# Kernel optimization log

Measured on AMD Instinct MI355X. Metric: run time of the kernel, lower is better.

## Reference

```python
import jax, jax.numpy as jnp
import numpy as np

M, NQ, NK, DX, H, HD, DT, KH = 2, 1024, 1024, 512, 8, 64, 2, 32
SCALE = HD ** -0.5


def setup_inputs() -> dict:
    key = jax.random.key(0)
    ks = jax.random.split(key, 12)
    w = lambda k, shape: jax.random.normal(k, shape, jnp.float32) * 0.02
    return dict(
        xq=jax.random.normal(ks[0], (M, NQ, DX), jnp.float32),
        xk=jax.random.normal(ks[1], (M, NK, DX), jnp.float32),
        xv=jax.random.normal(ks[2], (M, NK, DX), jnp.float32),
        tq=jax.random.normal(ks[3], (M, NQ, DT), jnp.float32),
        tk=jax.random.normal(ks[4], (M, NK, DT), jnp.float32),
        Wq=w(ks[5], (DX, H * HD)),
        Wk=w(ks[6], (DX, H * HD)),
        Wv=w(ks[7], (DX, H * HD)),
        Wo=w(ks[8], (H * HD, DX)),
        bo=jnp.zeros((DX,), jnp.float32),
        K1=w(ks[9], (DT, KH)),
        kb1=jnp.zeros((KH,), jnp.float32),
        K2=w(ks[10], (KH, H)),
        kb2=jnp.zeros((H,), jnp.float32),
    )


def _heads(t):
    # [b, n, h*d] -> [b, h, n, d]
    b, n, _ = t.shape
    return t.reshape(b, n, H, HD).transpose(0, 2, 1, 3)


def reference(xq, xk, xv, tq, tk, Wq, Wk, Wv, Wo, bo, K1, kb1, K2, kb2):
    q = _heads(xq @ Wq)            # [m,h,nq,d]
    k = _heads(xk @ Wk)            # [m,h,nk,d]
    token_dots = jnp.einsum('bhqd,bhkd->bhqk', q, k) * SCALE
    # diagonal attention term: query attends to its own (key/value-projected) token
    xq_k = _heads(xq @ Wk)
    diag_dots = jnp.sum(q * xq_k, axis=-1, keepdims=True) * SCALE   # [m,h,nq,1]
    token_dots = jnp.concatenate([token_dots, diag_dots], axis=-1)  # [m,h,nq,nk+1]
    # translation group action: pairwise differences, plus zero diagonal diff
    diff = tq[:, :, None, :] - tk[:, None, :, :]                    # [m,nq,nk,dt]
    diff = jnp.concatenate([diff, jnp.zeros((M, NQ, 1, DT), diff.dtype)], axis=2)
    # kernel network (MLP) -> per-head relative-position bias [m,nq,nk+1,h]
    kd = jax.nn.relu(diff @ K1 + kb1) @ K2 + kb2
    dots = token_dots + kd.transpose(0, 3, 1, 2)                    # [m,h,nq,nk+1]
    attn = jax.nn.softmax(dots, axis=-1)
    v = _heads(xv @ Wv)
    xq_v = _heads(xq @ Wv)
    out = jnp.einsum('bhqk,bhkd->bhqd', attn[..., :-1], v) + attn[..., -1:] * xq_v
    out = out.transpose(0, 2, 1, 3).reshape(M, NQ, H * HD) @ Wo + bo
    # phi_t is None -> tq_new = tq
    return (out, tq)
```

## Files before the change

kernel.cpp:

```cpp
#include <hip/hip_runtime.h>
#include <hip/hip_bf16.h>
#include <cstddef>

typedef __attribute__((ext_vector_type(8))) short bf16x8;
typedef __attribute__((ext_vector_type(4))) float f32x4;

constexpr int NH  = 8;
constexpr int HHD = 512;
constexpr int KHC = 32;
constexpr float SCALE_F = 0.125f;
constexpr int KSPLIT = 4;

__device__ __forceinline__ unsigned short f2bf(float f) {
    unsigned int u = __builtin_bit_cast(unsigned int, f);
    u = (u + 0x7FFFu + ((u >> 16) & 1u)) >> 16;
    return (unsigned short)u;
}
__device__ __forceinline__ float bf2f(unsigned short h) {
    unsigned int u = ((unsigned int)h) << 16;
    return __builtin_bit_cast(float, u);
}
__device__ __forceinline__ unsigned int cvt_pk_bf16(float lo, float hi) {
    unsigned int r;
    asm("v_cvt_pk_bf16_f32 %0, %1, %2" : "=v"(r) : "v"(lo), "v"(hi));
    return r;
}

struct PrepAll {
    const float* xs[3]; unsigned short* xd[3];
    const float* wsrc[4]; unsigned short* wdst[4];
    const float* tq; const float* tk;
    const float* K1; const float* kb1;
    float* Aa; float* Bb;
};
__global__ __launch_bounds__(256) void prep_all(PrepAll c) {
    __shared__ unsigned short Ts[64][66];
    const int b = blockIdx.x;
    const int t = threadIdx.x;

    if (b < 1536) {
        const int z = b / 512;
        const size_t i8 = ((size_t)(b - z * 512) * 256 + t) * 8;
        const float4 f0 = *(const float4*)(c.xs[z] + i8);
        const float4 f1 = *(const float4*)(c.xs[z] + i8 + 4);
        ushort4 o0, o1;
        o0.x = f2bf(f0.x); o0.y = f2bf(f0.y); o0.z = f2bf(f0.z); o0.w = f2bf(f0.w);
        o1.x = f2bf(f1.x); o1.y = f2bf(f1.y); o1.z = f2bf(f1.z); o1.w = f2bf(f1.w);
        *(ushort4*)(c.xd[z] + i8) = o0;
        *(ushort4*)(c.xd[z] + i8 + 4) = o1;
    } else if (b < 1792) {
        const int bb = b - 1536;
        const int z = bb >> 6;
        const int rem = bb & 63;
        const int k0 = (rem & 7) * 64, j0 = (rem >> 3) * 64;
        const float* W = c.wsrc[z];
        unsigned short* Wt = c.wdst[z];
        {
            const int kr = t >> 2;
            const int jc = (t & 3) * 16;
            const float* g = W + (size_t)(k0 + kr) * 512 + j0 + jc;
            #pragma unroll
            for (int i4 = 0; i4 < 4; ++i4) {
                float4 f = *(const float4*)(g + i4 * 4);
                Ts[kr][jc + i4 * 4 + 0] = f2bf(f.x);
                Ts[kr][jc + i4 * 4 + 1] = f2bf(f.y);
                Ts[kr][jc + i4 * 4 + 2] = f2bf(f.z);
                Ts[kr][jc + i4 * 4 + 3] = f2bf(f.w);
            }
        }
        __syncthreads();
        {
            const int j = t >> 2;
            const int kseg = (t & 3) * 16;
            unsigned short tmp[16];
            #pragma unroll
            for (int i = 0; i < 16; ++i) tmp[i] = Ts[kseg + i][j];
            unsigned short* g = Wt + (size_t)(j0 + j) * 512 + k0 + kseg;
            #pragma unroll
            for (int i4 = 0; i4 < 4; ++i4)
                *(ushort4*)(g + i4 * 4) = *(ushort4*)&tmp[i4 * 4];
        }
    } else {
        const int idx = (b - 1792) * 256 + t;
        const int which = idx >> 16;
        const int e = idx & 65535;
        const int row = e >> 5;
        const int j = e & 31;
        const float* tt = which ? c.tk : c.tq;
        float v = tt[row * 2 + 0] * c.K1[j] + tt[row * 2 + 1] * c.K1[KHC + j];
        if (!which) v += c.kb1[j];
        (which ? c.Bb : c.Aa)[e] = v;
    }
}

__device__ __forceinline__ void mfma_core_128(const unsigned short* __restrict__ A,
                                              const unsigned short* __restrict__ Bt,
                                              int r0, int c0, f32x4 acc[4][4])
{
    __shared__ __align__(16) char As[16384];
    __shared__ __align__(16) char Bs[16384];

    const int tid = threadIdx.x;
    const int l = tid & 63, w = tid >> 6;
    const int lw = l & 15, lg = l >> 4;
    const int wr = (w >> 1) * 64, wc = (w & 1) * 64;

    #pragma unroll
    for (int r = 0; r < 4; ++r)
        #pragma unroll
        for (int cb = 0; cb < 4; ++cb) acc[r][cb] = (f32x4){0.f, 0.f, 0.f, 0.f};

    const int row_s = tid >> 1;
    const int half  = tid & 1;

    for (int kb = 0; kb < 512; kb += 64) {
        __syncthreads();
        {
            const unsigned short* g = A + (size_t)(r0 + row_s) * 512 + kb + half * 32;
            const int base = row_s * 128 + half * 64;
            const int sw = (row_s & 7) << 4;
            #pragma unroll
            for (int i = 0; i < 4; ++i)
                *(float4*)(As + ((base + i * 16) ^ sw)) = *(const float4*)(g + i * 8);
        }
        {
            const unsigned short* g = Bt + (size_t)(c0 + row_s) * 512 + kb + half * 32;
            const int base = row_s * 128 + half * 64;
            const int sw = (row_s & 7) << 4;
            #pragma unroll
            for (int i = 0; i < 4; ++i)
                *(float4*)(Bs + ((base + i * 16) ^ sw)) = *(const float4*)(g + i * 8);
        }
        __syncthreads();

        bf16x8 bfrag[4][2];
        #pragma unroll
        for (int cb = 0; cb < 4; ++cb) {
            const int bcol = wc + cb * 16 + lw;
            const int sw = (bcol & 7) << 4;
            bfrag[cb][0] = *(const bf16x8*)(Bs + ((bcol * 128 + lg * 16) ^ sw));
            bfrag[cb][1] = *(const bf16x8*)(Bs + ((bcol * 128 + 64 + lg * 16) ^ sw));
        }
        #pragma unroll
        for (int r = 0; r < 4; ++r) {
            const int arow = wr + r * 16 + lw;
            const int sw = (arow & 7) << 4;
            bf16x8 a0 = *(const bf16x8*)(As + ((arow * 128 + lg * 16) ^ sw));
            bf16x8 a1 = *(const bf16x8*)(As + ((arow * 128 + 64 + lg * 16) ^ sw));
            #pragma unroll
            for (int cb = 0; cb < 4; ++cb) {
                acc[r][cb] = __builtin_amdgcn_mfma_f32_16x16x32_bf16(a0, bfrag[cb][0], acc[r][cb], 0, 0, 0);
                acc[r][cb] = __builtin_amdgcn_mfma_f32_16x16x32_bf16(a1, bfrag[cb][1], acc[r][cb], 0, 0, 0);
            }
        }
    }
}

struct ProjBias {
    const unsigned short* A[5];
    const unsigned short* B[5];
    unsigned short* O[5];
    unsigned short* VT;
    const float* Aa; const float* Bb;
    const float* K2; const float* kb2;
    unsigned short* kd;
};

__global__ __launch_bounds__(256) void projbias(ProjBias p) {
    const int b = blockIdx.x;
    const int tid = threadIdx.x;
    const int l = tid & 63;
    const int lw = l & 15, lg = l >> 4;

    if (b < 320) {
        const int z = b >> 6;
        const int t = b & 63;
        const int r0 = (t >> 2) * 128, c0 = (t & 3) * 128;
        f32x4 acc[4][4];
        mfma_core_128(p.A[z], p.B[z], r0, c0, acc);

        const int w = tid >> 6;
        const int wr = (w >> 1) * 64, wc = (w & 1) * 64;
        #pragma unroll
        for (int r = 0; r < 4; ++r)
            #pragma unroll
            for (int cb = 0; cb < 4; ++cb) {
                const int gc = c0 + wc + cb * 16 + lw;
                const int h = gc >> 6, d = gc & 63;
                #pragma unroll
                for (int rr = 0; rr < 4; ++rr) {
                    const int gr = r0 + wr + r * 16 + lg * 4 + rr;
                    const int m = gr >> 10, n = gr & 1023;
                    const unsigned short v = f2bf(acc[r][cb][rr]);
                    if (z == 2)
                        p.VT[(((size_t)m * NH + h) * 64 + d) * 1024 + n] = v;
                    else
                        p.O[z][(((size_t)m * NH + h) * 1024 + n) * 64 + d] = v;
                }
            }
    } else {
        const int bb = b - 320;
        const int kb = tid >> 6;
        const int kt = bb & 15;
        const int qg = (bb >> 4) & 63;
        const int m  = bb >> 10;

        float k2f[8];
        #pragma unroll
        for (int e = 0; e < 8; ++e)
            k2f[e] = (lw < 8) ? p.K2[(lg * 8 + e) * 8 + lw] : 0.f;
        union { unsigned int u[4]; bf16x8 v; } bu;
        #pragma unroll
        for (int i = 0; i < 4; ++i) bu.u[i] = cvt_pk_bf16(k2f[2 * i], k2f[2 * i + 1]);
        const bf16x8 bfrag = bu.v;

        const float c0v = (lw < 8) ? p.kb2[lw] : 0.f;
        const f32x4 cini = {c0v, c0v, c0v, c0v};

        const int kglob = kt * 64 + kb * 16 + lw;
        const float* bp = p.Bb + ((size_t)m * 1024 + kglob) * 32 + lg * 8;
        const float4 b0 = *(const float4*)bp;
        const float4 b1 = *(const float4*)(bp + 4);
        const float bl[8] = {b0.x, b0.y, b0.z, b0.w, b1.x, b1.y, b1.z, b1.w};

        const float* arow = p.Aa + ((size_t)m * 1024 + qg * 16) * 32 + lg * 8;
        unsigned short* kout = p.kd + (size_t)(m * 8 + lw) * 1048576
                             + qg * 16384 + kt * 1024 + kb * 256 + lg * 64;

        #pragma unroll
        for (int t = 0; t < 16; t += 2) {
            const float4 a00 = *(const float4*)(arow + (size_t)t * 32);
            const float4 a01 = *(const float4*)(arow + (size_t)t * 32 + 4);
            union { unsigned int u[4]; bf16x8 v; } r0u;
            r0u.u[0] = cvt_pk_bf16(fmaxf(a00.x - bl[0], 0.f), fmaxf(a00.y - bl[1], 0.f));
            r0u.u[1] = cvt_pk_bf16(fmaxf(a00.z - bl[2], 0.f), fmaxf(a00.w - bl[3], 0.f));
            r0u.u[2] = cvt_pk_bf16(fmaxf(a01.x - bl[4], 0.f), fmaxf(a01.y - bl[5], 0.f));
            r0u.u[3] = cvt_pk_bf16(fmaxf(a01.z - bl[6], 0.f), fmaxf(a01.w - bl[7], 0.f));
            const f32x4 d0 = __builtin_amdgcn_mfma_f32_16x16x32_bf16(r0u.v, bfrag, cini, 0, 0, 0);

            const float4 a10 = *(const float4*)(arow + (size_t)(t + 1) * 32);
            const float4 a11 = *(const float4*)(arow + (size_t)(t + 1) * 32 + 4);
            union { unsigned int u[4]; bf16x8 v; } r1u;
            r1u.u[0] = cvt_pk_bf16(fmaxf(a10.x - bl[0], 0.f), fmaxf(a10.y - bl[1], 0.f));
            r1u.u[1] = cvt_pk_bf16(fmaxf(a10.z - bl[2], 0.f), fmaxf(a10.w - bl[3], 0.f));
            r1u.u[2] = cvt_pk_bf16(fmaxf(a11.x - bl[4], 0.f), fmaxf(a11.y - bl[5], 0.f));
            r1u.u[3] = cvt_pk_bf16(fmaxf(a11.z - bl[6], 0.f), fmaxf(a11.w - bl[7], 0.f));
            const f32x4 d1 = __builtin_amdgcn_mfma_f32_16x16x32_bf16(r1u.v, bfrag, cini, 0, 0, 0);

            if (lw < 8) {
                uint4 o;
                o.x = cvt_pk_bf16(d0[0], d0[1]);
                o.y = cvt_pk_bf16(d0[2], d0[3]);
                o.z = cvt_pk_bf16(d1[0], d1[1]);
                o.w = cvt_pk_bf16(d1[2], d1[3]);
                *(uint4*)(kout + t * 4) = o;
            }
        }
    }
}

__global__ __launch_bounds__(256) void outproj_mfma(const unsigned short* __restrict__ A,
                                                    const unsigned short* __restrict__ Bt,
                                                    const float* __restrict__ bias,
                                                    float* __restrict__ C) {
    const int r0 = blockIdx.x * 128, c0 = blockIdx.y * 128;
    f32x4 acc[4][4];
    mfma_core_128(A, Bt, r0, c0, acc);

    const int l = threadIdx.x & 63, w = threadIdx.x >> 6;
    const int lw = l & 15, lg = l >> 4;
    const int wr = (w >> 1) * 64, wc = (w & 1) * 64;
    #pragma unroll
    for (int r = 0; r < 4; ++r)
        #pragma unroll
        for (int cb = 0; cb < 4; ++cb) {
            const int gc = c0 + wc + cb * 16 + lw;
            const float bv = bias[gc];
            #pragma unroll
            for (int rr = 0; rr < 4; ++rr) {
                const int gr = r0 + wr + r * 16 + lg * 4 + rr;
                C[(size_t)gr * HHD + gc] = acc[r][cb][rr] + bv;
            }
        }
}

__global__ __launch_bounds__(256, 4) void attn_mfma(
    const unsigned short* __restrict__ qh, const unsigned short* __restrict__ kh,
    const unsigned short* __restrict__ vt, const unsigned short* __restrict__ kd,
    float* __restrict__ pacc, float* __restrict__ pl)
{
    __shared__ __align__(16) char Ksh[8192];
    __shared__ __align__(16) char Vsh[8192];
    __shared__ __align__(16) char Psh[4][2048];

    const int tid = threadIdx.x;
    const int l = tid & 63;
    const int w = tid >> 6;
    const int lw = l & 15, lg = l >> 4;
    const int qt = blockIdx.x;
    const int mh = blockIdx.y;
    const int ks = blockIdx.z;
    const int q0 = qt * 64;

    const int qrow = q0 + w * 16 + lw;
    const unsigned short* qp = qh + ((size_t)mh * 1024 + qrow) * 64;
    const bf16x8 qf0 = *(const bf16x8*)(qp + lg * 8);
    const bf16x8 qf1 = *(const bf16x8*)(qp + 32 + lg * 8);

    f32x4 oacc[4] = {{0.f,0.f,0.f,0.f},{0.f,0.f,0.f,0.f},
                     {0.f,0.f,0.f,0.f},{0.f,0.f,0.f,0.f}};
    float lsum = 0.f;

    const int srow = tid >> 2;
    const int scol = (tid & 3) * 32;
    const int ssw  = (srow & 7) << 4;

    char* pbase = Psh[w];
    const int prsw = (lw & 7) << 4;
    const size_t kdwave = (((size_t)mh * 64 + qt * 4 + w) * 16 + ks * 4) * 1024;

    for (int kt = 0; kt < 4; ++kt) {
        const int k0 = ks * 256 + kt * 64;
        __syncthreads();
        {
            const char* g = (const char*)(kh + ((size_t)mh * 1024 + k0 + srow) * 64) + scol;
            const int a = srow * 128 + scol;
            *(float4*)(Ksh + (a ^ ssw))        = *(const float4*)g;
            *(float4*)(Ksh + ((a + 16) ^ ssw)) = *(const float4*)(g + 16);
        }
        {
            const char* g = (const char*)(vt + ((size_t)mh * 64 + srow) * 1024 + k0) + scol;
            const int a = srow * 128 + scol;
            *(float4*)(Vsh + (a ^ ssw))        = *(const float4*)g;
            *(float4*)(Vsh + ((a + 16) ^ ssw)) = *(const float4*)(g + 16);
        }
        __syncthreads();

        const unsigned short* kdt = kd + kdwave + (size_t)kt * 1024;
        #pragma unroll
        for (int kb = 0; kb < 4; ++kb) {
            f32x4 s = {0.f, 0.f, 0.f, 0.f};
            const int row = kb * 16 + lw;
            const int rsw = (row & 7) << 4;
            const int a0 = row * 128 + lg * 16;
            bf16x8 af0 = *(const bf16x8*)(Ksh + (a0 ^ rsw));
            s = __builtin_amdgcn_mfma_f32_16x16x32_bf16(af0, qf0, s, 0, 0, 0);
            bf16x8 af1 = *(const bf16x8*)(Ksh + ((a0 + 64) ^ rsw));
            s = __builtin_amdgcn_mfma_f32_16x16x32_bf16(af1, qf1, s, 0, 0, 0);

            ushort4 bb = *(const ushort4*)(kdt + kb * 256 + l * 4);
            float p0 = __expf(fmaf(s[0], SCALE_F, bf2f(bb.x)));
            float p1 = __expf(fmaf(s[1], SCALE_F, bf2f(bb.y)));
            float p2 = __expf(fmaf(s[2], SCALE_F, bf2f(bb.z)));
            float p3 = __expf(fmaf(s[3], SCALE_F, bf2f(bb.w)));
            lsum += (p0 + p1) + (p2 + p3);

            unsigned int u0 = f2bf(p0) | ((unsigned int)f2bf(p1) << 16);
            unsigned int u1 = f2bf(p2) | ((unsigned int)f2bf(p3) << 16);
            const int pa = lw * 128 + kb * 32 + lg * 8;
            *(uint2*)(pbase + (pa ^ prsw)) = make_uint2(u0, u1);
        }

        #pragma unroll
        for (int kc = 0; kc < 2; ++kc) {
            const int pa = lw * 128 + kc * 64 + lg * 16;
            bf16x8 pfrag = *(const bf16x8*)(pbase + (pa ^ prsw));
            #pragma unroll
            for (int db = 0; db < 4; ++db) {
                const int vrow = db * 16 + lw;
                const int va = vrow * 128 + kc * 64 + lg * 16;
                bf16x8 vfrag = *(const bf16x8*)(Vsh + (va ^ ((vrow & 7) << 4)));
                oacc[db] = __builtin_amdgcn_mfma_f32_16x16x32_bf16(pfrag, vfrag, oacc[db], 0, 0, 0);
            }
        }
    }

    lsum += __shfl_xor(lsum, 16, 64);
    lsum += __shfl_xor(lsum, 32, 64);

    float* pr = pacc + (((size_t)mh * KSPLIT + ks) * 1024) * 64;
    #pragma unroll
    for (int r = 0; r < 4; ++r) {
        const int qo = q0 + w * 16 + lg * 4 + r;
        float* rowp = pr + (size_t)qo * 64 + lw;
        rowp[0]  = oacc[0][r];
        rowp[16] = oacc[1][r];
        rowp[32] = oacc[2][r];
        rowp[48] = oacc[3][r];
    }
    if (lg == 0)
        pl[((size_t)mh * KSPLIT + ks) * 1024 + q0 + w * 16 + lw] = lsum;
}

__global__ __launch_bounds__(256) void reduce_k(
    const float* __restrict__ pacc, const float* __restrict__ pl,
    const unsigned short* __restrict__ qg, const unsigned short* __restrict__ xqk,
    const unsigned short* __restrict__ xqv, const float* __restrict__ K2,
    const float* __restrict__ kb1, const float* __restrict__ kb2,
    unsigned short* __restrict__ attn_out)
{
    const int rowid = blockIdx.x * 4 + (threadIdx.x >> 6);
    const int d = threadIdx.x & 63;
    const int mh = rowid >> 10;
    const int q = rowid & 1023;
    const int m = mh >> 3;
    const int h = mh & 7;

    float accsum = 0.f, lsumv = 0.f;
    #pragma unroll
    for (int kc = 0; kc < KSPLIT; ++kc) {
        accsum += pacc[(((size_t)mh * KSPLIT + kc) * 1024 + q) * 64 + d];
        lsumv  += pl[((size_t)mh * KSPLIT + kc) * 1024 + q];
    }
    const size_t ro = ((size_t)mh * 1024 + q) * 64 + d;
    float s = bf2f(qg[ro]) * bf2f(xqk[ro]);
    #pragma unroll
    for (int off = 32; off > 0; off >>= 1) s += __shfl_xor(s, off, 64);
    float bias_d = kb2[h];
    #pragma unroll
    for (int j = 0; j < KHC; ++j) bias_d += fmaxf(kb1[j], 0.f) * K2[j * NH + h];
    const float pd = __expf(fmaf(s, SCALE_F, bias_d));
    const float outv = (accsum + pd * bf2f(xqv[ro])) / (lsumv + pd);
    attn_out[((size_t)(m * 1024 + q)) * HHD + h * 64 + d] = f2bf(outv);
}

extern "C" void kernel_launch(void* const* d_in, const int* in_sizes, int n_in,
                              void* d_out, int out_size, void* d_ws, size_t ws_size,
                              hipStream_t stream)
{
    const float* xq  = (const float*)d_in[0];
    const float* xk  = (const float*)d_in[1];
    const float* xv  = (const float*)d_in[2];
    const float* tq  = (const float*)d_in[3];
    const float* tk  = (const float*)d_in[4];
    const float* Wq  = (const float*)d_in[5];
    const float* Wk  = (const float*)d_in[6];
    const float* Wv  = (const float*)d_in[7];
    const float* Wo  = (const float*)d_in[8];
    const float* bo  = (const float*)d_in[9];
    const float* K1  = (const float*)d_in[10];
    const float* kb1 = (const float*)d_in[11];
    const float* K2  = (const float*)d_in[12];
    const float* kb2 = (const float*)d_in[13];

    char* ws = (char*)d_ws;
    unsigned short* qh   = (unsigned short*)(ws);
    unsigned short* kh   = (unsigned short*)(ws +  2097152);
    unsigned short* vtp  = (unsigned short*)(ws +  4194304);
    unsigned short* xqk  = (unsigned short*)(ws +  6291456);
    unsigned short* xqv  = (unsigned short*)(ws +  8388608);
    float*          Aa   = (float*)(ws + 10485760);
    float*          Bb   = (float*)(ws + 10747904);
    unsigned short* kd   = (unsigned short*)(ws + 11010048);
    float*          pacc = (float*)(ws + 44564480);
    float*          pl   = (float*)(ws + 61341696);
    unsigned short* Wot  = (unsigned short*)(ws + 61603840);
    unsigned short* xa   = (unsigned short*)(ws + 11010048);
    unsigned short* xb   = (unsigned short*)(ws + 13107200);
    unsigned short* xc   = (unsigned short*)(ws + 15204352);
    unsigned short* Wqt  = (unsigned short*)(ws + 17301504);
    unsigned short* Wkt  = (unsigned short*)(ws + 17825792);
    unsigned short* Wvt  = (unsigned short*)(ws + 18350080);
    unsigned short* aout = (unsigned short*)(ws + 11010048);
    float*          outp = (float*)d_out;

    unsigned short* xa2  = (unsigned short*)(ws + 62128128);
    unsigned short* xb2  = (unsigned short*)(ws + 64225280);
    unsigned short* xc2  = (unsigned short*)(ws + 66322432);
    unsigned short* Wqt2 = (unsigned short*)(ws + 68419584);
    unsigned short* Wkt2 = (unsigned short*)(ws + 68943872);
    unsigned short* Wvt2 = (unsigned short*)(ws + 69468160);
    (void)xa; (void)xb; (void)xc; (void)Wqt; (void)Wkt; (void)Wvt;

    PrepAll pa;
    pa.xs[0] = xq; pa.xs[1] = xk; pa.xs[2] = xv;
    pa.xd[0] = xa2; pa.xd[1] = xb2; pa.xd[2] = xc2;
    pa.wsrc[0] = Wq; pa.wsrc[1] = Wk; pa.wsrc[2] = Wv; pa.wsrc[3] = Wo;
    pa.wdst[0] = Wqt2; pa.wdst[1] = Wkt2; pa.wdst[2] = Wvt2; pa.wdst[3] = Wot;
    pa.tq = tq; pa.tk = tk; pa.K1 = K1; pa.kb1 = kb1; pa.Aa = Aa; pa.Bb = Bb;
    hipLaunchKernelGGL(prep_all, dim3(2304), dim3(256), 0, stream, pa);

    ProjBias pb;
    pb.A[0] = xa2; pb.B[0] = Wqt2; pb.O[0] = qh;
    pb.A[1] = xb2; pb.B[1] = Wkt2; pb.O[1] = kh;
    pb.A[2] = xc2; pb.B[2] = Wvt2; pb.O[2] = nullptr;
    pb.A[3] = xa2; pb.B[3] = Wkt2; pb.O[3] = xqk;
    pb.A[4] = xa2; pb.B[4] = Wvt2; pb.O[4] = xqv;
    pb.VT = vtp;
    pb.Aa = Aa; pb.Bb = Bb; pb.K2 = K2; pb.kb2 = kb2; pb.kd = kd;
    hipLaunchKernelGGL(projbias, dim3(2368), dim3(256), 0, stream, pb);

    hipLaunchKernelGGL(attn_mfma, dim3(16, 16, KSPLIT), dim3(256), 0, stream,
                       qh, kh, vtp, kd, pacc, pl);

    hipLaunchKernelGGL(reduce_k, dim3(4096), dim3(256), 0, stream,
                       pacc, pl, qh, xqk, xqv, K2, kb1, kb2, aout);

    hipLaunchKernelGGL(outproj_mfma, dim3(16, 4, 1), dim3(256), 0, stream, aout, Wot, bo, outp);

    hipMemcpyAsync(outp + 1048576, tq, 4096 * sizeof(float),
                   hipMemcpyDeviceToDevice, stream);
}
```

Measured before the change: 159.1 us.

## Fuse split-K attention reduction into attention kernel with double-buffered K/V

```diff
diff --git a/kernel.cpp b/kernel.cpp
--- a/kernel.cpp
+++ b/kernel.cpp
@@ -9,7 +9,6 @@
 constexpr int HHD = 512;
 constexpr int KHC = 32;
 constexpr float SCALE_F = 0.125f;
-constexpr int KSPLIT = 4;
 
 __device__ __forceinline__ unsigned short f2bf(float f) {
     unsigned int u = __builtin_bit_cast(unsigned int, f);
@@ -284,25 +283,29 @@
         }
 }
 
-__global__ __launch_bounds__(256, 4) void attn_mfma(
+__global__ __launch_bounds__(512) void attn_fused(
     const unsigned short* __restrict__ qh, const unsigned short* __restrict__ kh,
     const unsigned short* __restrict__ vt, const unsigned short* __restrict__ kd,
-    float* __restrict__ pacc, float* __restrict__ pl)
+    const unsigned short* __restrict__ xqk, const unsigned short* __restrict__ xqv,
+    const float* __restrict__ K2, const float* __restrict__ kb1,
+    const float* __restrict__ kb2, unsigned short* __restrict__ aout)
 {
-    __shared__ __align__(16) char Ksh[8192];
-    __shared__ __align__(16) char Vsh[8192];
-    __shared__ __align__(16) char Psh[4][2048];
+    __shared__ __align__(16) char Ksh[2][8192];
+    __shared__ __align__(16) char Vsh[2][8192];
+    __shared__ __align__(16) char Psh[8][2048];
 
     const int tid = threadIdx.x;
+    const int w = tid >> 6;
+    const int half = w >> 2;
+    const int w4 = w & 3;
     const int l = tid & 63;
-    const int w = tid >> 6;
     const int lw = l & 15, lg = l >> 4;
     const int qt = blockIdx.x;
     const int mh = blockIdx.y;
-    const int ks = blockIdx.z;
+    const int m = mh >> 3, h = mh & 7;
     const int q0 = qt * 64;
 
-    const int qrow = q0 + w * 16 + lw;
+    const int qrow = q0 + w4 * 16 + lw;
     const unsigned short* qp = qh + ((size_t)mh * 1024 + qrow) * 64;
     const bf16x8 qf0 = *(const bf16x8*)(qp + lg * 8);
     const bf16x8 qf1 = *(const bf16x8*)(qp + 32 + lg * 8);
@@ -311,41 +314,57 @@
                      {0.f,0.f,0.f,0.f},{0.f,0.f,0.f,0.f}};
     float lsum = 0.f;
 
-    const int srow = tid >> 2;
-    const int scol = (tid & 3) * 32;
+    const int tid_h = tid & 255;
+    const int srow = tid_h >> 2;
+    const int scol = (tid_h & 3) * 32;
     const int ssw  = (srow & 7) << 4;
+    const int kbh  = half * 512;
+
+    __shared__ __align__(16) char Ksh2[2][2][8192];
+    __shared__ __align__(16) char Vsh2[2][2][8192];
 
     char* pbase = Psh[w];
     const int prsw = (lw & 7) << 4;
-    const size_t kdwave = (((size_t)mh * 64 + qt * 4 + w) * 16 + ks * 4) * 1024;
-
-    for (int kt = 0; kt < 4; ++kt) {
-        const int k0 = ks * 256 + kt * 64;
-        __syncthreads();
-        {
-            const char* g = (const char*)(kh + ((size_t)mh * 1024 + k0 + srow) * 64) + scol;
-            const int a = srow * 128 + scol;
-            *(float4*)(Ksh + (a ^ ssw))        = *(const float4*)g;
-            *(float4*)(Ksh + ((a + 16) ^ ssw)) = *(const float4*)(g + 16);
-        }
-        {
-            const char* g = (const char*)(vt + ((size_t)mh * 64 + srow) * 1024 + k0) + scol;
-            const int a = srow * 128 + scol;
-            *(float4*)(Vsh + (a ^ ssw))        = *(const float4*)g;
-            *(float4*)(Vsh + ((a + 16) ^ ssw)) = *(const float4*)(g + 16);
-        }
-        __syncthreads();
-
+    const size_t kdwave = (((size_t)mh * 64 + qt * 4 + w4) * 16 + half * 8) * 1024;
+
+    const char* kgbase = (const char*)(kh + ((size_t)mh * 1024 + kbh + srow) * 64) + scol;
+    const char* vgbase = (const char*)(vt + ((size_t)mh * 64 + srow) * 1024 + kbh) + scol;
+
+    float4 pk0, pk1, pv0, pv1;
+    #define PREFETCH(KT) do { \
+        const char* kg = kgbase + (size_t)(KT) * 8192; \
+        const char* vg = vgbase + (size_t)(KT) * 128; \
+        pk0 = *(const float4*)kg;  pk1 = *(const float4*)(kg + 16); \
+        pv0 = *(const float4*)vg;  pv1 = *(const float4*)(vg + 16); \
+    } while (0)
+    #define STAGE(BUF) do { \
+        const int a_ = srow * 128 + scol; \
+        *(float4*)(Ksh2[half][BUF] + (a_ ^ ssw))        = pk0; \
+        *(float4*)(Ksh2[half][BUF] + ((a_ + 16) ^ ssw)) = pk1; \
+        *(float4*)(Vsh2[half][BUF] + (a_ ^ ssw))        = pv0; \
+        *(float4*)(Vsh2[half][BUF] + ((a_ + 16) ^ ssw)) = pv1; \
+    } while (0)
+
+    PREFETCH(0);
+    STAGE(0);
+    __syncthreads();
+    PREFETCH(1);
+
+    for (int kt = 0; kt < 8; ++kt) {
+        const int buf = kt & 1;
+        const char* Kb = Ksh2[half][buf];
+        const char* Vb = Vsh2[half][buf];
         const unsigned short* kdt = kd + kdwave + (size_t)kt * 1024;
+
         #pragma unroll
         for (int kb = 0; kb < 4; ++kb) {
             f32x4 s = {0.f, 0.f, 0.f, 0.f};
             const int row = kb * 16 + lw;
             const int rsw = (row & 7) << 4;
             const int a0 = row * 128 + lg * 16;
-            bf16x8 af0 = *(const bf16x8*)(Ksh + (a0 ^ rsw));
+            bf16x8 af0 = *(const bf16x8*)(Kb + (a0 ^ rsw));
             s = __builtin_amdgcn_mfma_f32_16x16x32_bf16(af0, qf0, s, 0, 0, 0);
-            bf16x8 af1 = *(const bf16x8*)(Ksh + ((a0 + 64) ^ rsw));
+            bf16x8 af1 = *(const bf16x8*)(Kb + ((a0 + 64) ^ rsw));
             s = __builtin_amdgcn_mfma_f32_16x16x32_bf16(af1, qf1, s, 0, 0, 0);
 
             ushort4 bb = *(const ushort4*)(kdt + kb * 256 + l * 4);
@@ -369,59 +388,76 @@
             for (int db = 0; db < 4; ++db) {
                 const int vrow = db * 16 + lw;
                 const int va = vrow * 128 + kc * 64 + lg * 16;
-                bf16x8 vfrag = *(const bf16x8*)(Vsh + (va ^ ((vrow & 7) << 4)));
+                bf16x8 vfrag = *(const bf16x8*)(Vb + (va ^ ((vrow & 7) << 4)));
                 oacc[db] = __builtin_amdgcn_mfma_f32_16x16x32_bf16(pfrag, vfrag, oacc[db], 0, 0, 0);
             }
         }
+
+        if (kt < 7) {
+            STAGE((kt + 1) & 1);
+            if (kt < 6) PREFETCH(kt + 2);
+            __syncthreads();
+        }
     }
+    #undef PREFETCH
+    #undef STAGE
 
     lsum += __shfl_xor(lsum, 16, 64);
     lsum += __shfl_xor(lsum, 32, 64);
 
-    float* pr = pacc + (((size_t)mh * KSPLIT + ks) * 1024) * 64;
-    #pragma unroll
-    for (int r = 0; r < 4; ++r) {
-        const int qo = q0 + w * 16 + lg * 4 + r;
-        float* rowp = pr + (size_t)qo * 64 + lw;
-        rowp[0]  = oacc[0][r];
-        rowp[16] = oacc[1][r];
-        rowp[32] = oacc[2][r];
-        rowp[48] = oacc[3][r];
+    __syncthreads();
+    float* exch  = (float*)&Ksh[0][0];
+    float* exchl = (float*)&Vsh[0][0];
+    if (half == 1) {
+        #pragma unroll
+        for (int r = 0; r < 4; ++r)
+            #pragma unroll
+            for (int db = 0; db < 4; ++db)
+                exch[w4 * 1024 + (lg * 4 + r) * 64 + db * 16 + lw] = oacc[db][r];
+        if (lg == 0) exchl[w4 * 16 + lw] = lsum;
     }
-    if (lg == 0)
-        pl[((size_t)mh * KSPLIT + ks) * 1024 + q0 + w * 16 + lw] = lsum;
-}
-
-__global__ __launch_bounds__(256) void reduce_k(
-    const float* __restrict__ pacc, const float* __restrict__ pl,
-    const unsigned short* __restrict__ qg, const unsigned short* __restrict__ xqk,
-    const unsigned short* __restrict__ xqv, const float* __restrict__ K2,
-    const float* __restrict__ kb1, const float* __restrict__ kb2,
-    unsigned short* __restrict__ attn_out)
-{
-    const int rowid = blockIdx.x * 4 + (threadIdx.x >> 6);
-    const int d = threadIdx.x & 63;
-    const int mh = rowid >> 10;
-    const int q = rowid & 1023;
-    const int m = mh >> 3;
-    const int h = mh & 7;
-
-    float accsum = 0.f, lsumv = 0.f;
-    #pragma unroll
-    for (int kc = 0; kc < KSPLIT; ++kc) {
-        accsum += pacc[(((size_t)mh * KSPLIT + kc) * 1024 + q) * 64 + d];
-        lsumv  += pl[((size_t)mh * KSPLIT + kc) * 1024 + q];
+    __syncthreads();
+    if (half == 0) {
+        #pragma unroll
+        for (int r = 0; r < 4; ++r)
+            #pragma unroll
+            for (int db = 0; db < 4; ++db)
+                oacc[db][r] += exch[w4 * 1024 + (lg * 4 + r) * 64 + db * 16 + lw];
+        lsum += exchl[w4 * 16 + lw];
+
+        const unsigned short* xkp = xqk + ((size_t)mh * 1024 + qrow) * 64;
+        const bf16x8 xf0 = *(const bf16x8*)(xkp + lg * 8);
+        const bf16x8 xf1 = *(const bf16x8*)(xkp + 32 + lg * 8);
+        float sd = 0.f;
+        #pragma unroll
+        for (int j = 0; j < 8; ++j) {
+            sd = fmaf(bf2f((unsigned short)qf0[j]), bf2f((unsigned short)xf0[j]), sd);
+            sd = fmaf(bf2f((unsigned short)qf1[j]), bf2f((unsigned short)xf1[j]), sd);
+        }
+        sd += __shfl_xor(sd, 16, 64);
+        sd += __shfl_xor(sd, 32, 64);
+        float biasd = kb2[h];
+        #pragma unroll
+        for (int j = 0; j < KHC; ++j)
+            biasd += fmaxf(kb1[j], 0.f) * K2[j * NH + h];
+        const float pd = __expf(fmaf(sd, SCALE_F, biasd));
+        const float denom = lsum + pd;
+
+        #pragma unroll
+        for (int r = 0; r < 4; ++r) {
+            const int qq = lg * 4 + r;
+            const float pdq = __shfl(pd, qq, 64);
+            const float inv = 1.f / __shfl(denom, qq, 64);
+            const int qr2 = q0 + w4 * 16 + qq;
+            const unsigned short* xv = xqv + ((size_t)mh * 1024 + qr2) * 64;
+            unsigned short* ao = aout + ((size_t)(m * 1024 + qr2)) * HHD + h * 64;
+            #pragma unroll
+            for (int db = 0; db < 4; ++db) {
+                const int d = db * 16 + lw;
+                ao[d] = f2bf((oacc[db][r] + pdq * bf2f(xv[d])) * inv);
+            }
+        }
     }
-    const size_t ro = ((size_t)mh * 1024 + q) * 64 + d;
-    float s = bf2f(qg[ro]) * bf2f(xqk[ro]);
-    #pragma unroll
-    for (int off = 32; off > 0; off >>= 1) s += __shfl_xor(s, off, 64);
-    float bias_d = kb2[h];
-    #pragma unroll
-    for (int j = 0; j < KHC; ++j) bias_d += fmaxf(kb1[j], 0.f) * K2[j * NH + h];
-    const float pd = __expf(fmaf(s, SCALE_F, bias_d));
-    const float outv = (accsum + pd * bf2f(xqv[ro])) / (lsumv + pd);
-    attn_out[((size_t)(m * 1024 + q)) * HHD + h * 64 + d] = f2bf(outv);
 }
 
 extern "C" void kernel_launch(void* const* d_in, const int* in_sizes, int n_in,
@@ -452,25 +488,15 @@
     float*          Aa   = (float*)(ws + 10485760);
     float*          Bb   = (float*)(ws + 10747904);
     unsigned short* kd   = (unsigned short*)(ws + 11010048);
-    float*          pacc = (float*)(ws + 44564480);
-    float*          pl   = (float*)(ws + 61341696);
+    unsigned short* aout = (unsigned short*)(ws + 44564480);
     unsigned short* Wot  = (unsigned short*)(ws + 61603840);
-    unsigned short* xa   = (unsigned short*)(ws + 11010048);
-    unsigned short* xb   = (unsigned short*)(ws + 13107200);
-    unsigned short* xc   = (unsigned short*)(ws + 15204352);
-    unsigned short* Wqt  = (unsigned short*)(ws + 17301504);
-    unsigned short* Wkt  = (unsigned short*)(ws + 17825792);
-    unsigned short* Wvt  = (unsigned short*)(ws + 18350080);
-    unsigned short* aout = (unsigned short*)(ws + 11010048);
-    float*          outp = (float*)d_out;
-
     unsigned short* xa2  = (unsigned short*)(ws + 62128128);
     unsigned short* xb2  = (unsigned short*)(ws + 64225280);
     unsigned short* xc2  = (unsigned short*)(ws + 66322432);
     unsigned short* Wqt2 = (unsigned short*)(ws + 68419584);
     unsigned short* Wkt2 = (unsigned short*)(ws + 68943872);
     unsigned short* Wvt2 = (unsigned short*)(ws + 69468160);
-    (void)xa; (void)xb; (void)xc; (void)Wqt; (void)Wkt; (void)Wvt;
+    float*          outp = (float*)d_out;
 
     PrepAll pa;
     pa.xs[0] = xq; pa.xs[1] = xk; pa.xs[2] = xv;
@@ -490,11 +516,8 @@
     pb.Aa = Aa; pb.Bb = Bb; pb.K2 = K2; pb.kb2 = kb2; pb.kd = kd;
     hipLaunchKernelGGL(projbias, dim3(2368), dim3(256), 0, stream, pb);
 
-    hipLaunchKernelGGL(attn_mfma, dim3(16, 16, KSPLIT), dim3(256), 0, stream,
-                       qh, kh, vtp, kd, pacc, pl);
-
-    hipLaunchKernelGGL(reduce_k, dim3(4096), dim3(256), 0, stream,
-                       pacc, pl, qh, xqk, xqv, K2, kb1, kb2, aout);
+    hipLaunchKernelGGL(attn_fused, dim3(16, 16), dim3(512), 0, stream,
+                       qh, kh, vtp, kd, xqk, xqv, K2, kb1, kb2, aout);
 
     hipLaunchKernelGGL(outproj_mfma, dim3(16, 4, 1), dim3(256), 0, stream, aout, Wot, bo, outp);
 
```

Measured after the change: 152.2 us. 4.4% less time.
